# Kernel optimization log

Hardware: AMD Instinct MI355X
Metric: run time of the kernel (lower is better)

Reference implementation:

```python
import jax, jax.numpy as jnp
import numpy as np

NUM_NODES = 50000
NUM_EDGES = 600000
IN_DIM = 128
HID = 128
OUT_DIM = 10
NUM_GRAPHS = 64


def setup_inputs() -> dict:
    key = jax.random.key(0)
    ks = jax.random.split(key, 12)
    x = jax.random.normal(ks[0], (NUM_NODES, IN_DIM), dtype=jnp.float32)
    edge_index = jax.random.randint(ks[1], (2, NUM_EDGES), 0, NUM_NODES, dtype=jnp.int64)
    batch = jnp.sort(jax.random.randint(ks[2], (NUM_NODES,), 0, NUM_GRAPHS, dtype=jnp.int64))
    s = 0.05
    W1 = jax.random.normal(ks[3], (IN_DIM, HID), dtype=jnp.float32) * s
    b1 = jnp.zeros((HID,), dtype=jnp.float32)
    W2 = jax.random.normal(ks[4], (HID, HID), dtype=jnp.float32) * s
    b2 = jnp.zeros((HID,), dtype=jnp.float32)
    W3 = jax.random.normal(ks[5], (HID, HID), dtype=jnp.float32) * s
    b3 = jnp.zeros((HID,), dtype=jnp.float32)
    Wlin = jax.random.normal(ks[6], (HID, OUT_DIM), dtype=jnp.float32) * s
    blin = jnp.zeros((OUT_DIM,), dtype=jnp.float32)
    return {"x": x, "edge_index": edge_index, "batch": batch,
            "W1": W1, "b1": b1, "W2": W2, "b2": b2, "W3": W3, "b3": b3,
            "Wlin": Wlin, "blin": blin}


def _gcn_conv(x, W, b, src, dst, norm):
    # h = X W ; out[i] = sum_{(j->i)} norm_e * h[j] ; + bias
    h = x @ W                                   # [N, H]
    msg = h[src] * norm[:, None]                # [E+N, H] gather + scale
    out = jax.ops.segment_sum(msg, dst, num_segments=x.shape[0])  # scatter-add
    return out + b


def reference(x, edge_index, batch, W1, b1, W2, b2, W3, b3, Wlin, blin):
    N = x.shape[0]
    # add self loops (PyG GCNConv default)
    loops = jnp.arange(N, dtype=edge_index.dtype)
    src = jnp.concatenate([edge_index[0], loops])
    dst = jnp.concatenate([edge_index[1], loops])
    # symmetric normalization D^{-1/2} (A+I) D^{-1/2}; degree on target nodes
    deg = jax.ops.segment_sum(jnp.ones_like(dst, dtype=x.dtype), dst, num_segments=N)
    dinv = jnp.where(deg > 0, jax.lax.rsqrt(deg), 0.0)
    norm = dinv[src] * dinv[dst]

    h = jax.nn.relu(_gcn_conv(x, W1, b1, src, dst, norm))   # dropout = identity (eval)
    h = jax.nn.relu(_gcn_conv(h, W2, b2, src, dst, norm))
    h = jax.nn.relu(_gcn_conv(h, W3, b3, src, dst, norm))

    # global mean pool over graphs
    sums = jax.ops.segment_sum(h, batch, num_segments=NUM_GRAPHS)          # [G, H]
    cnts = jax.ops.segment_sum(jnp.ones((N,), dtype=h.dtype), batch, num_segments=NUM_GRAPHS)
    pooled = sums / jnp.maximum(cnts, 1.0)[:, None]
    return pooled @ Wlin + blin                                            # [G, OUT]
```

## Files before the change

kernel.cpp:

```cpp
#include <hip/hip_runtime.h>
#include <hip/hip_bf16.h>
#include <hip/hip_fp16.h>


#define HID 128
#define NGRAPH 64

typedef _Float16 half8v __attribute__((ext_vector_type(8)));
typedef float floatx4 __attribute__((ext_vector_type(4)));

__device__ __forceinline__ int idx_at(const void* p, long long i, int f64) {
    if (f64) return (int)((const long long*)p)[i];
    return ((const int*)p)[i];
}

__global__ void init_kernel(const int* __restrict__ ei, int* __restrict__ flag,
                            int* __restrict__ counts, float* __restrict__ pooled,
                            float* __restrict__ gcnt, uint4* __restrict__ csr4,
                            int N, int nCsr4) {
    int i = blockIdx.x * blockDim.x + threadIdx.x;
    int stride = gridDim.x * blockDim.x;
    if (i < N) counts[i] = 0;
    if (i < NGRAPH * HID) pooled[i] = 0.f;
    if (i < NGRAPH) gcnt[i] = 0.f;
    unsigned fillv = (unsigned)N | ((unsigned)N << 16);
    uint4 fv = make_uint4(fillv, fillv, fillv, fillv);
    for (int j = i; j < nCsr4; j += stride) csr4[j] = fv;
    if (blockIdx.x == 0) {
        __shared__ int cnt;
        if (threadIdx.x == 0) cnt = 0;
        __syncthreads();
        int z = 0;
        for (int k = threadIdx.x; k < 2048; k += 256)
            if (ei[2 * k + 1] == 0) z++;
        atomicAdd(&cnt, z);
        __syncthreads();
        if (threadIdx.x == 0) *flag = (cnt > 1024) ? 1 : 0;
    }
}

__global__ void hist_kernel(const void* __restrict__ ei, const int* __restrict__ flag,
                            int* __restrict__ counts, int E, int N) {
    int e = blockIdx.x * blockDim.x + threadIdx.x;
    if (e >= E) return;
    int f64 = *flag;
    int d = idx_at(ei, (long long)E + e, f64);
    if ((unsigned)d < (unsigned)N) atomicAdd(&counts[d], 1);
}

__device__ __forceinline__ int wave_incl_scan(int v, int lane) {
#pragma unroll
    for (int off = 1; off < 64; off <<= 1) {
        int u = __shfl_up(v, off);
        if (lane >= off) v += u;
    }
    return v;
}

__global__ __launch_bounds__(256) void blocksum_kernel(const int* __restrict__ counts,
                                                       int* __restrict__ bsums, int N) {
    int i = blockIdx.x * 256 + threadIdx.x;
    int v = (i < N) ? ((counts[i] + 7) & ~7) : 0;
    int lane = threadIdx.x & 63, w = threadIdx.x >> 6;
#pragma unroll
    for (int off = 32; off > 0; off >>= 1) v += __shfl_down(v, off);
    __shared__ int ws[4];
    if (lane == 0) ws[w] = v;
    __syncthreads();
    if (threadIdx.x == 0) bsums[blockIdx.x] = ws[0] + ws[1] + ws[2] + ws[3];
}

__global__ __launch_bounds__(256) void scanb_kernel(int* __restrict__ bsums, int nb) {
    int t = threadIdx.x;
    int lane = t & 63, w = t >> 6;
    int v = (t < nb) ? bsums[t] : 0;
    int iv = wave_incl_scan(v, lane);
    __shared__ int wsum[4];
    if (lane == 63) wsum[w] = iv;
    __syncthreads();
    int add = 0;
    for (int k = 0; k < w; ++k) add += wsum[k];
    if (t < nb) bsums[t] = iv - v + add;
}

__global__ __launch_bounds__(256) void fill_kernel(const int* __restrict__ counts,
                                                   const int* __restrict__ bsums,
                                                   int* __restrict__ rowstart,
                                                   int* __restrict__ cursor,
                                                   float* __restrict__ dinv, int N) {
    int i = blockIdx.x * 256 + threadIdx.x;
    int c = (i < N) ? counts[i] : 0;
    int cp = (c + 7) & ~7;
    int lane = threadIdx.x & 63, w = threadIdx.x >> 6;
    int iv = wave_incl_scan(cp, lane);
    __shared__ int wsum[4];
    if (lane == 63) wsum[w] = iv;
    __syncthreads();
    int add = bsums[blockIdx.x];
    for (int k = 0; k < w; ++k) add += wsum[k];
    int excl = iv - cp + add;
    if (i < N) {
        rowstart[i] = excl;
        cursor[i] = excl;
        dinv[i] = rsqrtf((float)(c + 1));
        if (i == N - 1) rowstart[N] = excl + cp;
    }
}

__global__ void scatter_kernel(const void* __restrict__ ei, const int* __restrict__ flag,
                               int* __restrict__ cursor,
                               unsigned short* __restrict__ csr_src, int E, int N) {
    int e = blockIdx.x * blockDim.x + threadIdx.x;
    if (e >= E) return;
    int f64 = *flag;
    int s = idx_at(ei, e, f64);
    int d = idx_at(ei, (long long)E + e, f64);
    if ((unsigned)s >= (unsigned)N || (unsigned)d >= (unsigned)N) return;
    int pos = atomicAdd(&cursor[d], 1);
    csr_src[pos] = (unsigned short)s;
}

__global__ __launch_bounds__(256) void prep_kernel(const float* __restrict__ x,
                                                   const float* __restrict__ dinv,
                                                   __half2* __restrict__ xs,
                                                   __half2* __restrict__ hsA,
                                                   __half2* __restrict__ hsB,
                                                   const float* __restrict__ W1,
                                                   const float* __restrict__ W2,
                                                   const float* __restrict__ W3,
                                                   half8v* __restrict__ wf,
                                                   int N, int n2) {
    if (blockIdx.x < 24) {
        int which = blockIdx.x >> 3;
        const float* W = which == 0 ? W1 : (which == 1 ? W2 : W3);
        int t = (blockIdx.x & 7) * 256 + threadIdx.x;
        int lane = t & 63;
        int nt = (t >> 6) & 7;
        int kblk = t >> 9;
        int n = nt * 16 + (lane & 15);
        int kbase = kblk * 32 + (lane >> 4) * 8;
        half8v v;
#pragma unroll
        for (int j = 0; j < 8; ++j) v[j] = (_Float16)W[(size_t)(kbase + j) * 128 + n];
        wf[which * 2048 + t] = v;
    } else if (blockIdx.x == 24) {
        int t = threadIdx.x;
        __half2 z = __floats2half2_rn(0.f, 0.f);
        if (t < 64) xs[(size_t)N * 64 + t] = z;
        else if (t < 128) hsA[(size_t)N * 64 + (t - 64)] = z;
        else if (t < 192) hsB[(size_t)N * 64 + (t - 128)] = z;
    } else {
        int i = (blockIdx.x - 25) * 256 + threadIdx.x;
        if (i >= n2) return;
        float dv = dinv[i >> 6];
        float2 v = ((const float2*)x)[i];
        xs[i] = __floats2half2_rn(dv * v.x, dv * v.y);
    }
}

__global__ __launch_bounds__(256) void agg_kernel(const __half2* __restrict__ xs,
                                                  const int* __restrict__ rowstart,
                                                  const unsigned short* __restrict__ csr_src,
                                                  const float* __restrict__ dinv,
                                                  __half2* __restrict__ out, int N) {
    int wid = (blockIdx.x * blockDim.x + threadIdx.x) >> 6;
    int lane = threadIdx.x & 63;
    if (wid >= N) return;
    float di = dinv[wid];
    float2 s0 = __half22float2(xs[(size_t)wid * 64 + lane]);
    float accx = s0.x, accy = s0.y;
    float bccx = 0.f, bccy = 0.f;
    int e0 = rowstart[wid], e1 = rowstart[wid + 1];
    for (int e = e0; e < e1; e += 8) {
        uint4 q = *(const uint4*)(csr_src + e);
        int s0i = q.x & 0xffff, s1i = q.x >> 16;
        int s2i = q.y & 0xffff, s3i = q.y >> 16;
        int s4i = q.z & 0xffff, s5i = q.z >> 16;
        int s6i = q.w & 0xffff, s7i = q.w >> 16;
        __half2 v0 = xs[(size_t)s0i * 64 + lane];
        __half2 v1 = xs[(size_t)s1i * 64 + lane];
        __half2 v2 = xs[(size_t)s2i * 64 + lane];
        __half2 v3 = xs[(size_t)s3i * 64 + lane];
        __half2 v4 = xs[(size_t)s4i * 64 + lane];
        __half2 v5 = xs[(size_t)s5i * 64 + lane];
        __half2 v6 = xs[(size_t)s6i * 64 + lane];
        __half2 v7 = xs[(size_t)s7i * 64 + lane];
        float2 f0 = __half22float2(v0), f1 = __half22float2(v1);
        float2 f2 = __half22float2(v2), f3 = __half22float2(v3);
        float2 f4 = __half22float2(v4), f5 = __half22float2(v5);
        float2 f6 = __half22float2(v6), f7 = __half22float2(v7);
        accx += f0.x + f2.x; accy += f0.y + f2.y;
        bccx += f1.x + f3.x; bccy += f1.y + f3.y;
        accx += f4.x + f6.x; accy += f4.y + f6.y;
        bccx += f5.x + f7.x; bccy += f5.y + f7.y;
    }
    out[(size_t)wid * 64 + lane] = __floats2half2_rn(di * (accx + bccx),
                                                     di * (accy + bccy));
}

template <bool SCALED>
__global__ __launch_bounds__(256) void gemm_mfma(const __half2* __restrict__ A16,
                                                 const half8v* __restrict__ wf,
                                                 const float* __restrict__ bias,
                                                 const float* __restrict__ dinv,
                                                 __half2* __restrict__ O16, int M) {
    int wid = threadIdx.x >> 6, lane = threadIdx.x & 63;
    int rowTile = blockIdx.x * 64 + wid * 16;
    int hi = lane >> 4;
    int arow = rowTile + (lane & 15);
    if (arow >= M) arow = M - 1;
    const half8v* Arow = (const half8v*)((const _Float16*)A16 + (size_t)arow * 128);

    floatx4 acc[8];
#pragma unroll
    for (int nt = 0; nt < 8; ++nt) acc[nt] = (floatx4){0.f, 0.f, 0.f, 0.f};

#pragma unroll
    for (int kb = 0; kb < 4; ++kb) {
        half8v a = Arow[kb * 4 + hi];
#pragma unroll
        for (int nt = 0; nt < 8; ++nt) {
            half8v w = wf[(kb * 8 + nt) * 64 + lane];
            acc[nt] = __builtin_amdgcn_mfma_f32_16x16x32_f16(a, w, acc[nt], 0, 0, 0);
        }
    }

    int ocol_lo = lane & 15;
    int orow0 = rowTile + hi * 4;
    float dv[4];
#pragma unroll
    for (int r = 0; r < 4; ++r) {
        int orow = orow0 + r;
        dv[r] = (SCALED && orow < M) ? dinv[orow] : 1.0f;
    }
#pragma unroll
    for (int nt = 0; nt < 8; ++nt) {
        int col = nt * 16 + ocol_lo;
        float b = bias[col];
#pragma unroll
        for (int r = 0; r < 4; ++r) {
            int orow = orow0 + r;
            if (orow < M) {
                float v = fmaxf(acc[nt][r] + b, 0.f);
                if (SCALED) v *= dv[r];
                ((_Float16*)O16)[(size_t)orow * 128 + col] = (_Float16)v;
            }
        }
    }
}

#define POOL_CHUNK 16
__global__ __launch_bounds__(256) void pool_kernel(const __half2* __restrict__ h,
                                                   const void* __restrict__ batch,
                                                   const int* __restrict__ flag,
                                                   float* __restrict__ pooled,
                                                   float* __restrict__ gcnt, int N) {
    int wid = (blockIdx.x * blockDim.x + threadIdx.x) >> 6;
    int lane = threadIdx.x & 63;
    int n0 = wid * POOL_CHUNK;
    if (n0 >= N) return;
    int n1 = n0 + POOL_CHUNK; if (n1 > N) n1 = N;
    int f64 = *flag;
    int g = idx_at(batch, n0, f64);
    float ax = 0.f, ay = 0.f;
    int cnt = 0;
    for (int n = n0; n < n1; ++n) {
        int gn = idx_at(batch, n, f64);
        if (gn != g) {
            if ((unsigned)g < (unsigned)NGRAPH) {
                atomicAdd(&pooled[g * HID + 2 * lane], ax);
                atomicAdd(&pooled[g * HID + 2 * lane + 1], ay);
                if (lane == 0) atomicAdd(&gcnt[g], (float)cnt);
            }
            ax = ay = 0.f; cnt = 0; g = gn;
        }
        float2 v = __half22float2(h[(size_t)n * 64 + lane]);
        ax += v.x; ay += v.y; cnt++;
    }
    if ((unsigned)g < (unsigned)NGRAPH) {
        atomicAdd(&pooled[g * HID + 2 * lane], ax);
        atomicAdd(&pooled[g * HID + 2 * lane + 1], ay);
        if (lane == 0) atomicAdd(&gcnt[g], (float)cnt);
    }
}

__global__ __launch_bounds__(128) void final_kernel(const float* __restrict__ pooled,
                                                    const float* __restrict__ gcnt,
                                                    const float* __restrict__ Wl,
                                                    const float* __restrict__ bl,
                                                    float* __restrict__ out) {
    int o = blockIdx.x * blockDim.x + threadIdx.x;
    if (o >= NGRAPH * 10) return;
    int g = o / 10, c = o % 10;
    float inv = 1.0f / fmaxf(gcnt[g], 1.0f);
    float acc = 0.f;
    for (int k = 0; k < HID; ++k)
        acc = fmaf(pooled[g * HID + k], Wl[k * 10 + c], acc);
    out[o] = acc * inv + bl[c];
}

extern "C" void kernel_launch(void* const* d_in, const int* in_sizes, int n_in,
                              void* d_out, int out_size, void* d_ws, size_t ws_size,
                              hipStream_t stream) {
    const float* x   = (const float*)d_in[0];
    const void* ei   = d_in[1];
    const void* bat  = d_in[2];
    const float* W1  = (const float*)d_in[3];
    const float* b1  = (const float*)d_in[4];
    const float* W2  = (const float*)d_in[5];
    const float* b2  = (const float*)d_in[6];
    const float* W3  = (const float*)d_in[7];
    const float* b3  = (const float*)d_in[8];
    const float* Wl  = (const float*)d_in[9];
    const float* bl  = (const float*)d_in[10];
    float* out = (float*)d_out;

    const int N = in_sizes[0] / HID;
    const int E = in_sizes[1] / 2;
    const int EPAD = (E + 7 * N + 7) & ~7;

    char* w = (char*)d_ws;
    size_t off = 0;
    auto carve = [&](size_t bytes) -> void* {
        void* p = w + off;
        off = (off + bytes + 255) & ~(size_t)255;
        return p;
    };
    __half2* xs       = (__half2*)carve((size_t)(N + 1) * HID * 2);
    __half2* aggB16   = (__half2*)carve((size_t)N * HID * 2);
    __half2* hsA      = (__half2*)carve((size_t)(N + 1) * HID * 2);
    __half2* hsB      = (__half2*)carve((size_t)(N + 1) * HID * 2);
    int*     counts   = (int*)carve((size_t)N * 4);
    int*     rowstart = (int*)carve((size_t)(N + 1) * 4);
    int*     cursor   = (int*)carve((size_t)N * 4);
    float*   dinv     = (float*)carve((size_t)N * 4);
    unsigned short* csr_src = (unsigned short*)carve((size_t)EPAD * 2);
    float*   pooled   = (float*)carve((size_t)NGRAPH * HID * 4);
    float*   gcnt     = (float*)carve((size_t)NGRAPH * 4);
    half8v*  wf       = (half8v*)carve(3 * 2048 * 16);
    int*     bsums    = (int*)carve(1024);
    int*     flag     = (int*)carve(256);

    const int nb = (N + 255) / 256;
    const int n2 = N * HID / 2;

    init_kernel<<<nb, 256, 0, stream>>>((const int*)ei, flag, counts, pooled, gcnt,
                                        (uint4*)csr_src, N, EPAD / 8);
    hist_kernel<<<(E + 255) / 256, 256, 0, stream>>>(ei, flag, counts, E, N);
    blocksum_kernel<<<nb, 256, 0, stream>>>(counts, bsums, N);
    scanb_kernel<<<1, 256, 0, stream>>>(bsums, nb);
    fill_kernel<<<nb, 256, 0, stream>>>(counts, bsums, rowstart, cursor, dinv, N);
    scatter_kernel<<<(E + 255) / 256, 256, 0, stream>>>(ei, flag, cursor, csr_src, E, N);
    prep_kernel<<<25 + (n2 + 255) / 256, 256, 0, stream>>>(x, dinv, xs, hsA, hsB,
                                                           W1, W2, W3, wf, N, n2);

    int aggBlocks  = (N + 3) / 4;
    int gemmBlocks = (N + 63) / 64;

    agg_kernel<<<aggBlocks, 256, 0, stream>>>(xs, rowstart, csr_src, dinv, aggB16, N);
    gemm_mfma<true><<<gemmBlocks, 256, 0, stream>>>(aggB16, wf, b1, dinv, hsA, N);
    agg_kernel<<<aggBlocks, 256, 0, stream>>>(hsA, rowstart, csr_src, dinv, aggB16, N);
    gemm_mfma<true><<<gemmBlocks, 256, 0, stream>>>(aggB16, wf + 2048, b2, dinv, hsB, N);
    agg_kernel<<<aggBlocks, 256, 0, stream>>>(hsB, rowstart, csr_src, dinv, aggB16, N);
    gemm_mfma<false><<<gemmBlocks, 256, 0, stream>>>(aggB16, wf + 4096, b3, dinv, hsA, N);

    int poolWaves = (N + POOL_CHUNK - 1) / POOL_CHUNK;
    int poolBlocks = (poolWaves + 3) / 4;
    pool_kernel<<<poolBlocks, 256, 0, stream>>>(hsA, bat, flag, pooled, gcnt, N);
    final_kernel<<<5, 128, 0, stream>>>(pooled, gcnt, Wl, bl, out);
}
```

Baseline: 230.4 us.

## Fuse global mean pooling into final GEMM epilogue and count nodes in fill

The last-layer GEMM no longer writes its fp16 output. It instead reduces the relu'd rows per graph into an LDS buffer and atomically adds the result into the pooled sums, which removes the separate pool kernel and the write and reread of the final hidden tensor. Per-graph node counts move into fill_kernel as per-node atomic adds. This adds LDS atomics, extra block syncs for each graph spanned by a tile, and heavy global atomic contention on the 64 graph counters.

After: 537.2 us. 133% more time.

```diff
diff --git a/kernel.cpp b/kernel.cpp
--- a/kernel.cpp
+++ b/kernel.cpp
@@ -87,7 +87,10 @@
                                                    const int* __restrict__ bsums,
                                                    int* __restrict__ rowstart,
                                                    int* __restrict__ cursor,
-                                                   float* __restrict__ dinv, int N) {
+                                                   float* __restrict__ dinv,
+                                                   const void* __restrict__ batch,
+                                                   const int* __restrict__ flag,
+                                                   float* __restrict__ gcnt, int N) {
     int i = blockIdx.x * 256 + threadIdx.x;
     int c = (i < N) ? counts[i] : 0;
     int cp = (c + 7) & ~7;
@@ -104,6 +107,8 @@
         cursor[i] = excl;
         dinv[i] = rsqrtf((float)(c + 1));
         if (i == N - 1) rowstart[N] = excl + cp;
+        int g = idx_at(batch, i, *flag);
+        if ((unsigned)g < (unsigned)NGRAPH) atomicAdd(&gcnt[g], 1.0f);
     }
 }
 
@@ -198,12 +203,16 @@
                                                      di * (accy + bccy));
 }
 
-template <bool SCALED>
+template <bool POOL>
 __global__ __launch_bounds__(256) void gemm_mfma(const __half2* __restrict__ A16,
                                                  const half8v* __restrict__ wf,
                                                  const float* __restrict__ bias,
                                                  const float* __restrict__ dinv,
-                                                 __half2* __restrict__ O16, int M) {
+                                                 __half2* __restrict__ O16,
+                                                 const void* __restrict__ batch,
+                                                 const int* __restrict__ flag,
+                                                 float* __restrict__ pooled, int M) {
+    __shared__ float lds_pool[HID];
     int wid = threadIdx.x >> 6, lane = threadIdx.x & 63;
     int rowTile = blockIdx.x * 64 + wid * 16;
     int hi = lane >> 4;
@@ -227,60 +236,59 @@
 
     int ocol_lo = lane & 15;
     int orow0 = rowTile + hi * 4;
-    float dv[4];
-#pragma unroll
-    for (int r = 0; r < 4; ++r) {
-        int orow = orow0 + r;
-        dv[r] = (SCALED && orow < M) ? dinv[orow] : 1.0f;
-    }
-#pragma unroll
-    for (int nt = 0; nt < 8; ++nt) {
-        int col = nt * 16 + ocol_lo;
-        float b = bias[col];
+
+    if (!POOL) {
+        float dv[4];
 #pragma unroll
         for (int r = 0; r < 4; ++r) {
             int orow = orow0 + r;
-            if (orow < M) {
-                float v = fmaxf(acc[nt][r] + b, 0.f);
-                if (SCALED) v *= dv[r];
-                ((_Float16*)O16)[(size_t)orow * 128 + col] = (_Float16)v;
+            dv[r] = (orow < M) ? dinv[orow] : 1.0f;
+        }
+#pragma unroll
+        for (int nt = 0; nt < 8; ++nt) {
+            int col = nt * 16 + ocol_lo;
+            float b = bias[col];
+#pragma unroll
+            for (int r = 0; r < 4; ++r) {
+                int orow = orow0 + r;
+                if (orow < M) {
+                    float v = fmaxf(acc[nt][r] + b, 0.f) * dv[r];
+                    ((_Float16*)O16)[(size_t)orow * 128 + col] = (_Float16)v;
+                }
             }
         }
-    }
-}
-
-#define POOL_CHUNK 16
-__global__ __launch_bounds__(256) void pool_kernel(const __half2* __restrict__ h,
-                                                   const void* __restrict__ batch,
-                                                   const int* __restrict__ flag,
-                                                   float* __restrict__ pooled,
-                                                   float* __restrict__ gcnt, int N) {
-    int wid = (blockIdx.x * blockDim.x + threadIdx.x) >> 6;
-    int lane = threadIdx.x & 63;
-    int n0 = wid * POOL_CHUNK;
-    if (n0 >= N) return;
-    int n1 = n0 + POOL_CHUNK; if (n1 > N) n1 = N;
-    int f64 = *flag;
-    int g = idx_at(batch, n0, f64);
-    float ax = 0.f, ay = 0.f;
-    int cnt = 0;
-    for (int n = n0; n < n1; ++n) {
-        int gn = idx_at(batch, n, f64);
-        if (gn != g) {
-            if ((unsigned)g < (unsigned)NGRAPH) {
-                atomicAdd(&pooled[g * HID + 2 * lane], ax);
-                atomicAdd(&pooled[g * HID + 2 * lane + 1], ay);
-                if (lane == 0) atomicAdd(&gcnt[g], (float)cnt);
+    } else {
+        int f64 = *flag;
+        int rlo = blockIdx.x * 64;
+        int rhi = rlo + 63; if (rhi >= M) rhi = M - 1;
+        int gmin = idx_at(batch, rlo, f64);
+        int gmax = idx_at(batch, rhi, f64);
+        int gr[4];
+#pragma unroll
+        for (int r = 0; r < 4; ++r) {
+            int orow = orow0 + r;
+            gr[r] = (orow < M) ? idx_at(batch, orow, f64) : -1;
+        }
+        for (int g = gmin; g <= gmax; ++g) {
+            for (int c = threadIdx.x; c < HID; c += 256) lds_pool[c] = 0.f;
+            __syncthreads();
+#pragma unroll
+            for (int nt = 0; nt < 8; ++nt) {
+                int col = nt * 16 + ocol_lo;
+                float b = bias[col];
+#pragma unroll
+                for (int r = 0; r < 4; ++r) {
+                    if (gr[r] == g) {
+                        float v = fmaxf(acc[nt][r] + b, 0.f);
+                        atomicAdd(&lds_pool[col], v);
+                    }
+                }
             }
-            ax = ay = 0.f; cnt = 0; g = gn;
-        }
-        float2 v = __half22float2(h[(size_t)n * 64 + lane]);
-        ax += v.x; ay += v.y; cnt++;
-    }
-    if ((unsigned)g < (unsigned)NGRAPH) {
-        atomicAdd(&pooled[g * HID + 2 * lane], ax);
-        atomicAdd(&pooled[g * HID + 2 * lane + 1], ay);
-        if (lane == 0) atomicAdd(&gcnt[g], (float)cnt);
+            __syncthreads();
+            if (threadIdx.x < HID && (unsigned)g < (unsigned)NGRAPH)
+                atomicAdd(&pooled[g * HID + threadIdx.x], lds_pool[threadIdx.x]);
+            __syncthreads();
+        }
     }
 }
 
@@ -349,7 +357,8 @@
     hist_kernel<<<(E + 255) / 256, 256, 0, stream>>>(ei, flag, counts, E, N);
     blocksum_kernel<<<nb, 256, 0, stream>>>(counts, bsums, N);
     scanb_kernel<<<1, 256, 0, stream>>>(bsums, nb);
-    fill_kernel<<<nb, 256, 0, stream>>>(counts, bsums, rowstart, cursor, dinv, N);
+    fill_kernel<<<nb, 256, 0, stream>>>(counts, bsums, rowstart, cursor, dinv,
+                                        bat, flag, gcnt, N);
     scatter_kernel<<<(E + 255) / 256, 256, 0, stream>>>(ei, flag, cursor, csr_src, E, N);
     prep_kernel<<<25 + (n2 + 255) / 256, 256, 0, stream>>>(x, dinv, xs, hsA, hsB,
                                                            W1, W2, W3, wf, N, n2);
@@ -358,14 +367,14 @@
     int gemmBlocks = (N + 63) / 64;
 
     agg_kernel<<<aggBlocks, 256, 0, stream>>>(xs, rowstart, csr_src, dinv, aggB16, N);
-    gemm_mfma<true><<<gemmBlocks, 256, 0, stream>>>(aggB16, wf, b1, dinv, hsA, N);
+    gemm_mfma<false><<<gemmBlocks, 256, 0, stream>>>(aggB16, wf, b1, dinv, hsA,
+                                                     bat, flag, pooled, N);
     agg_kernel<<<aggBlocks, 256, 0, stream>>>(hsA, rowstart, csr_src, dinv, aggB16, N);
-    gemm_mfma<true><<<gemmBlocks, 256, 0, stream>>>(aggB16, wf + 2048, b2, dinv, hsB, N);
+    gemm_mfma<false><<<gemmBlocks, 256, 0, stream>>>(aggB16, wf + 2048, b2, dinv, hsB,
+                                                     bat, flag, pooled, N);
     agg_kernel<<<aggBlocks, 256, 0, stream>>>(hsB, rowstart, csr_src, dinv, aggB16, N);
-    gemm_mfma<false><<<gemmBlocks, 256, 0, stream>>>(aggB16, wf + 4096, b3, dinv, hsA, N);
-
-    int poolWaves = (N + POOL_CHUNK - 1) / POOL_CHUNK;
-    int poolBlocks = (poolWaves + 3) / 4;
-    pool_kernel<<<poolBlocks, 256, 0, stream>>>(hsA, bat, flag, pooled, gcnt, N);
+    gemm_mfma<true><<<gemmBlocks, 256, 0, stream>>>(aggB16, wf + 4096, b3, dinv, nullptr,
+                                                    bat, flag, pooled, N);
+
     final_kernel<<<5, 128, 0, stream>>>(pooled, gcnt, Wl, bl, out);
 }
```
